# Kernel tuning notes

Hardware: AMD Instinct MI355X
Metric: run time of the kernel (lower is better)

## Reference

```python
import jax, jax.numpy as jnp
import numpy as np

HIDDEN = 2048
NUM_HEADS = 16
HEAD_DIM = HIDDEN // NUM_HEADS
ROPE_THETA = 10000.0


def _rope_cos_sin(n, dtype):
    # Llama-style: inv_freq over even indices, emb = concat([freqs, freqs])
    inv_freq = 1.0 / (ROPE_THETA ** (jnp.arange(0, HEAD_DIM, 2, dtype=jnp.float32) / HEAD_DIM))
    pos = jnp.arange(n, dtype=jnp.float32)
    freqs = pos[:, None] * inv_freq[None, :]          # [N, HEAD_DIM/2]
    emb = jnp.concatenate([freqs, freqs], axis=-1)    # [N, HEAD_DIM]
    return jnp.cos(emb).astype(dtype), jnp.sin(emb).astype(dtype)


def _rotate_half(x):
    x1, x2 = jnp.split(x, 2, axis=-1)
    return jnp.concatenate([-x2, x1], axis=-1)


def setup_inputs() -> dict:
    key = jax.random.key(0)
    ks = jax.random.split(key, 5)
    B, N, D = 2, 2048, HIDDEN
    s = 1.0 / np.sqrt(D)
    return {
        "x": jax.random.normal(ks[0], (B, N, D), jnp.float32),
        "Wq": jax.random.normal(ks[1], (D, D), jnp.float32) * s,
        "Wk": jax.random.normal(ks[2], (D, D), jnp.float32) * s,
        "Wv": jax.random.normal(ks[3], (D, D), jnp.float32) * s,
        "Wo": jax.random.normal(ks[4], (D, D), jnp.float32) * s,
    }


def reference(x, Wq, Wk, Wv, Wo):
    B, N, D = x.shape
    scale = HEAD_DIM ** -0.5

    def proj(W):  # nn.Linear(bias=False): x @ W.T, then split heads -> [B,H,N,hd]
        return (x @ W.T).reshape(B, N, NUM_HEADS, HEAD_DIM).transpose(0, 2, 1, 3)

    q, k, v = proj(Wq), proj(Wk), proj(Wv)

    cos, sin = _rope_cos_sin(N, x.dtype)  # [N, HEAD_DIM]
    cos = cos[None, None]                 # broadcast over B, H
    sin = sin[None, None]
    q = q * cos + _rotate_half(q) * sin
    k = k * cos + _rotate_half(k) * sin

    attn = jnp.einsum("bhqd,bhkd->bhqk", q, k) * scale  # full N x N scores
    attn = jax.nn.softmax(attn, axis=-1)                 # dropout p=0 -> identity
    out = jnp.einsum("bhqk,bhkd->bhqd", attn, v)
    out = out.transpose(0, 2, 1, 3).reshape(B, N, D)
    return out @ Wo.T
```

## Files before the change

### kernel.cpp

```cpp
#include <hip/hip_runtime.h>
#include <hip/hip_bf16.h>
#include <math.h>

typedef short bf16x8 __attribute__((ext_vector_type(8)));
typedef short bf16x4 __attribute__((ext_vector_type(4)));
typedef float f32x4 __attribute__((ext_vector_type(4)));

#define NSEQ 2048
#define DMODEL 2048
#define NH 16
#define HD 128
#define BATCH 2
#define MROWS 4096

__device__ __forceinline__ unsigned short f2b(float f) {
    __hip_bfloat16 h = __float2bfloat16(f);
    return *reinterpret_cast<unsigned short*>(&h);
}
__device__ __forceinline__ float b2f(unsigned short u) {
    __hip_bfloat16 h;
    *reinterpret_cast<unsigned short*>(&h) = u;
    return __bfloat162float(h);
}

__device__ __forceinline__ void gld_lds16(const unsigned short* g, unsigned short* l) {
    __builtin_amdgcn_global_load_lds(
        (const __attribute__((address_space(1))) unsigned int*)(const void*)g,
        (__attribute__((address_space(3))) unsigned int*)(void*)l,
        16, 0, 0);
}

__global__ __launch_bounds__(256) void cast_all_kernel(const float* __restrict__ x,
                                                       const float* __restrict__ wq,
                                                       const float* __restrict__ wk,
                                                       const float* __restrict__ wv,
                                                       const float* __restrict__ wo,
                                                       unsigned short* __restrict__ xb,
                                                       unsigned short* __restrict__ wqb) {
    int bid = blockIdx.x;
    const float* src;
    unsigned short* dst;
    int off;
    if (bid < 4096) {
        src = x; dst = xb; off = bid;
    } else {
        int w = (bid - 4096) >> 11;
        src = (w == 0) ? wq : (w == 1) ? wk : (w == 2) ? wv : wo;
        dst = wqb + (size_t)w * 4194304;
        off = (bid - 4096) & 2047;
    }
    int i = (off * 256 + threadIdx.x) * 8;
    float4 a = *(const float4*)(src + i);
    float4 b = *(const float4*)(src + i + 4);
    union { unsigned short u[8]; uint4 v; } tmp;
    tmp.u[0] = f2b(a.x); tmp.u[1] = f2b(a.y); tmp.u[2] = f2b(a.z); tmp.u[3] = f2b(a.w);
    tmp.u[4] = f2b(b.x); tmp.u[5] = f2b(b.y); tmp.u[6] = f2b(b.z); tmp.u[7] = f2b(b.w);
    *(uint4*)(dst + i) = tmp.v;
}

__global__ __launch_bounds__(256) void gemm_qkv(const unsigned short* __restrict__ A,
                                                const unsigned short* __restrict__ Bw,
                                                unsigned short* __restrict__ qk,
                                                unsigned short* __restrict__ vt) {
    __shared__ unsigned short sA[128 * 32];
    __shared__ unsigned short sB[128 * 32];
    const int K = DMODEL;
    const int tid = threadIdx.x;
    const int wave = tid >> 6, lane = tid & 63;
    const int m0 = blockIdx.y * 128, n0 = blockIdx.x * 128;
    const int wm = (wave >> 1) * 64, wn = (wave & 1) * 64;

    f32x4 acc[4][4] = {};

    const int srow = wave * 32 + (lane >> 2);
    const int scol = (lane & 3) * 8;
    const unsigned short* Ag = A + (size_t)(m0 + srow) * K + scol;
    const unsigned short* Bg = Bw + (size_t)(n0 + srow) * K + scol;
    unsigned short* sA0 = &sA[(wave * 32) * 32];
    unsigned short* sA1 = &sA[(wave * 32 + 16) * 32];
    unsigned short* sB0 = &sB[(wave * 32) * 32];
    unsigned short* sB1 = &sB[(wave * 32 + 16) * 32];
    const int fr = lane & 15, fo = (lane >> 4) * 8;

    for (int kb = 0; kb < K; kb += 32) {
        gld_lds16(Ag + kb, sA0);
        gld_lds16(Ag + (size_t)16 * K + kb, sA1);
        gld_lds16(Bg + kb, sB0);
        gld_lds16(Bg + (size_t)16 * K + kb, sB1);
        __syncthreads();
        bf16x8 af[4], bfr[4];
        #pragma unroll
        for (int mt = 0; mt < 4; mt++)
            af[mt] = *(const bf16x8*)&sA[(wm + mt * 16 + fr) * 32 + fo];
        #pragma unroll
        for (int nt = 0; nt < 4; nt++)
            bfr[nt] = *(const bf16x8*)&sB[(wn + nt * 16 + fr) * 32 + fo];
        #pragma unroll
        for (int mt = 0; mt < 4; mt++)
            #pragma unroll
            for (int nt = 0; nt < 4; nt++)
                acc[mt][nt] = __builtin_amdgcn_mfma_f32_16x16x32_bf16(af[mt], bfr[nt], acc[mt][nt], 0, 0, 0);
        __syncthreads();
    }

    const int g4 = (lane >> 4) * 4, c0 = lane & 15;
    if (n0 < 4096) {
        #pragma unroll
        for (int mt = 0; mt < 4; mt++)
            #pragma unroll
            for (int nt = 0; nt < 4; nt++) {
                int col = n0 + wn + nt * 16 + c0;
                size_t base = (size_t)(col >> 11) * 8388608 + (size_t)(col & 2047);
                #pragma unroll
                for (int r = 0; r < 4; r++) {
                    int row = m0 + wm + mt * 16 + g4 + r;
                    qk[base + (size_t)row * 2048] = f2b(acc[mt][nt][r]);
                }
            }
    } else {
        #pragma unroll
        for (int mt = 0; mt < 4; mt++) {
            int mbase = m0 + wm + mt * 16 + g4;
            int bb = mbase >> 11;
            int nn = mbase & 2047;
            #pragma unroll
            for (int nt = 0; nt < 4; nt++) {
                int d = n0 - 4096 + wn + nt * 16 + c0;
                union { unsigned short u[4]; uint2 v; } o;
                #pragma unroll
                for (int r = 0; r < 4; r++) o.u[r] = f2b(acc[mt][nt][r]);
                *(uint2*)(vt + ((size_t)(bb * 2048 + d)) * 2048 + nn) = o.v;
            }
        }
    }
}

__global__ __launch_bounds__(256) void gemm_out(const unsigned short* __restrict__ A,
                                                const unsigned short* __restrict__ Bw,
                                                float* __restrict__ Cf) {
    __shared__ unsigned short sA[128 * 32];
    __shared__ unsigned short sB[128 * 32];
    const int K = DMODEL, Nn = DMODEL;
    const int tid = threadIdx.x;
    const int wave = tid >> 6, lane = tid & 63;
    const int m0 = blockIdx.y * 128, n0 = blockIdx.x * 128;
    const int wm = (wave >> 1) * 64, wn = (wave & 1) * 64;

    f32x4 acc[4][4] = {};

    const int srow = wave * 32 + (lane >> 2);
    const int scol = (lane & 3) * 8;
    const unsigned short* Ag = A + (size_t)(m0 + srow) * K + scol;
    const unsigned short* Bg = Bw + (size_t)(n0 + srow) * K + scol;
    unsigned short* sA0 = &sA[(wave * 32) * 32];
    unsigned short* sA1 = &sA[(wave * 32 + 16) * 32];
    unsigned short* sB0 = &sB[(wave * 32) * 32];
    unsigned short* sB1 = &sB[(wave * 32 + 16) * 32];
    const int fr = lane & 15, fo = (lane >> 4) * 8;

    for (int kb = 0; kb < K; kb += 32) {
        gld_lds16(Ag + kb, sA0);
        gld_lds16(Ag + (size_t)16 * K + kb, sA1);
        gld_lds16(Bg + kb, sB0);
        gld_lds16(Bg + (size_t)16 * K + kb, sB1);
        __syncthreads();
        bf16x8 af[4], bfr[4];
        #pragma unroll
        for (int mt = 0; mt < 4; mt++)
            af[mt] = *(const bf16x8*)&sA[(wm + mt * 16 + fr) * 32 + fo];
        #pragma unroll
        for (int nt = 0; nt < 4; nt++)
            bfr[nt] = *(const bf16x8*)&sB[(wn + nt * 16 + fr) * 32 + fo];
        #pragma unroll
        for (int mt = 0; mt < 4; mt++)
            #pragma unroll
            for (int nt = 0; nt < 4; nt++)
                acc[mt][nt] = __builtin_amdgcn_mfma_f32_16x16x32_bf16(af[mt], bfr[nt], acc[mt][nt], 0, 0, 0);
        __syncthreads();
    }

    const int g4 = (lane >> 4) * 4, c0 = lane & 15;
    #pragma unroll
    for (int mt = 0; mt < 4; mt++)
        #pragma unroll
        for (int nt = 0; nt < 4; nt++) {
            int col = n0 + wn + nt * 16 + c0;
            #pragma unroll
            for (int r = 0; r < 4; r++) {
                int row = m0 + wm + mt * 16 + g4 + r;
                Cf[(size_t)row * Nn + col] = acc[mt][nt][r];
            }
        }
}

__global__ __launch_bounds__(256) void rope_kernel(unsigned short* __restrict__ Q,
                                                   unsigned short* __restrict__ Kb) {
    int t = blockIdx.x * 256 + threadIdx.x;
    int dq = t & 15, h = (t >> 4) & 15, m = t >> 8;
    int n = m & (NSEQ - 1);
    size_t base = (size_t)m * DMODEL + h * HD + dq * 4;

    union U4 { unsigned short u[4]; uint2 v; };
    U4 qlo, qhi, klo, khi, oql, oqh, okl, okh;
    qlo.v = *(const uint2*)(Q + base);
    qhi.v = *(const uint2*)(Q + base + 64);
    klo.v = *(const uint2*)(Kb + base);
    khi.v = *(const uint2*)(Kb + base + 64);

    const float scq = 0.08838834764831845f;
    #pragma unroll
    for (int j = 0; j < 4; j++) {
        int d = dq * 4 + j;
        float invf = exp2f((float)d * -0.2076205059304545f);
        float fr = (float)n * invf;
        float sv, cv;
        __sincosf(fr, &sv, &cv);
        float q1 = b2f(qlo.u[j]), q2 = b2f(qhi.u[j]);
        float k1 = b2f(klo.u[j]), k2 = b2f(khi.u[j]);
        oql.u[j] = f2b((q1 * cv - q2 * sv) * scq);
        oqh.u[j] = f2b((q2 * cv + q1 * sv) * scq);
        okl.u[j] = f2b(k1 * cv - k2 * sv);
        okh.u[j] = f2b(k2 * cv + k1 * sv);
    }
    *(uint2*)(Q + base)       = oql.v;
    *(uint2*)(Q + base + 64)  = oqh.v;
    *(uint2*)(Kb + base)      = okl.v;
    *(uint2*)(Kb + base + 64) = okh.v;
}

__global__ __launch_bounds__(256) void attn_kernel(const unsigned short* __restrict__ Q,
                                                   const unsigned short* __restrict__ Kg,
                                                   const unsigned short* __restrict__ Vt,
                                                   unsigned short* __restrict__ O) {
    __shared__ unsigned short sK[64 * 136];
    __shared__ unsigned short sV[128 * 88];

    const int bh = blockIdx.x;
    const int b = bh >> 4, h = bh & 15;
    const int qt = blockIdx.y;
    const int tid = threadIdx.x, wave = tid >> 6, lane = tid & 63;
    const int c0 = lane & 15, grp = lane >> 4;

    bf16x8 qf[2][4];
    {
        const unsigned short* Qbase = Q + (size_t)(b * NSEQ + qt * 128 + wave * 32 + c0) * DMODEL + h * HD + grp * 8;
        #pragma unroll
        for (int nt = 0; nt < 2; nt++)
            #pragma unroll
            for (int ks = 0; ks < 4; ks++)
                qf[nt][ks] = *(const bf16x8*)(Qbase + (size_t)nt * 16 * DMODEL + ks * 32);
    }

    f32x4 oacc[8][2] = {};
    float lsum[2] = {0.f, 0.f};

    const unsigned short* Kbase = Kg + (size_t)(b * NSEQ) * DMODEL + h * HD;
    const unsigned short* Vbase = Vt + (size_t)(bh * HD) * NSEQ;

    for (int kv0 = 0; kv0 < NSEQ; kv0 += 64) {
        __syncthreads();
        #pragma unroll
        for (int i = 0; i < 4; i++) {
            int fl = i * 256 + tid;
            int rr = fl >> 4, cc = fl & 15;
            *(uint4*)&sK[rr * 136 + cc * 8] = *(const uint4*)(Kbase + (size_t)(kv0 + rr) * DMODEL + cc * 8);
        }
        #pragma unroll
        for (int i = 0; i < 4; i++) {
            int fl = i * 256 + tid;
            int rr = fl >> 3, cc = fl & 7;
            *(uint4*)&sV[rr * 88 + cc * 8] = *(const uint4*)(Vbase + (size_t)rr * NSEQ + kv0 + cc * 8);
        }
        __syncthreads();

        f32x4 s[4][2] = {};
        #pragma unroll
        for (int ks = 0; ks < 4; ks++) {
            bf16x8 kf[4];
            #pragma unroll
            for (int mt = 0; mt < 4; mt++)
                kf[mt] = *(const bf16x8*)&sK[(mt * 16 + c0) * 136 + ks * 32 + grp * 8];
            #pragma unroll
            for (int mt = 0; mt < 4; mt++)
                #pragma unroll
                for (int nt = 0; nt < 2; nt++)
                    s[mt][nt] = __builtin_amdgcn_mfma_f32_16x16x32_bf16(kf[mt], qf[nt][ks], s[mt][nt], 0, 0, 0);
        }

        bf16x4 pk[4][2];
        #pragma unroll
        for (int mt = 0; mt < 4; mt++)
            #pragma unroll
            for (int nt = 0; nt < 2; nt++) {
                float p0 = __expf(s[mt][nt][0]);
                float p1 = __expf(s[mt][nt][1]);
                float p2 = __expf(s[mt][nt][2]);
                float p3 = __expf(s[mt][nt][3]);
                lsum[nt] += (p0 + p1) + (p2 + p3);
                bf16x4 t;
                t[0] = (short)f2b(p0); t[1] = (short)f2b(p1);
                t[2] = (short)f2b(p2); t[3] = (short)f2b(p3);
                pk[mt][nt] = t;
            }

        #pragma unroll
        for (int mtK = 0; mtK < 4; mtK++) {
            bf16x4 va[8];
            #pragma unroll
            for (int mo = 0; mo < 8; mo++)
                va[mo] = *(const bf16x4*)&sV[(mo * 16 + c0) * 88 + mtK * 16 + grp * 4];
            #pragma unroll
            for (int mo = 0; mo < 8; mo++)
                #pragma unroll
                for (int nt = 0; nt < 2; nt++)
                    oacc[mo][nt] = __builtin_amdgcn_mfma_f32_16x16x16bf16_1k(va[mo], pk[mtK][nt], oacc[mo][nt], 0, 0, 0);
        }
    }

    float invl[2];
    #pragma unroll
    for (int nt = 0; nt < 2; nt++) {
        float li = lsum[nt];
        li += __shfl_xor(li, 16);
        li += __shfl_xor(li, 32);
        invl[nt] = 1.0f / li;
    }
    #pragma unroll
    for (int mo = 0; mo < 8; mo++)
        #pragma unroll
        for (int nt = 0; nt < 2; nt++) {
            union { unsigned short u[4]; uint2 v; } o;
            #pragma unroll
            for (int r = 0; r < 4; r++)
                o.u[r] = f2b(oacc[mo][nt][r] * invl[nt]);
            int row = b * NSEQ + qt * 128 + wave * 32 + nt * 16 + c0;
            int col = h * HD + mo * 16 + grp * 4;
            *(uint2*)(O + (size_t)row * DMODEL + col) = o.v;
        }
}

extern "C" void kernel_launch(void* const* d_in, const int* in_sizes, int n_in,
                              void* d_out, int out_size, void* d_ws, size_t ws_size,
                              hipStream_t stream) {
    const float* x  = (const float*)d_in[0];
    const float* Wq = (const float*)d_in[1];
    const float* Wk = (const float*)d_in[2];
    const float* Wv = (const float*)d_in[3];
    const float* Wo = (const float*)d_in[4];

    char* ws = (char*)d_ws;
    unsigned short* xb  = (unsigned short*)(ws);
    unsigned short* wqb = (unsigned short*)(ws + 16777216);
    unsigned short* wob = (unsigned short*)(ws + 16777216 + 3 * 8388608);
    unsigned short* qb  = (unsigned short*)(ws + 50331648);
    unsigned short* kb  = (unsigned short*)(ws + 67108864);
    unsigned short* vt  = (unsigned short*)(ws + 83886080);

    cast_all_kernel<<<12288, 256, 0, stream>>>(x, Wq, Wk, Wv, Wo, xb, wqb);

    gemm_qkv<<<dim3(48, 32), 256, 0, stream>>>(xb, wqb, qb, vt);

    rope_kernel<<<4096, 256, 0, stream>>>(qb, kb);

    attn_kernel<<<dim3(32, 16), 256, 0, stream>>>(qb, kb, vt, xb);

    gemm_out<<<dim3(16, 32), 256, 0, stream>>>(xb, wob, (float*)d_out);
}
```

Before: 423.1 us.

## Fuse RoPE into QKV GEMM epilogue and shrink output GEMM M-tile

The QKV GEMM now gives each wave a full 128-column head slice (2x8 MFMA tiles), so the lo/hi halves needed by rotate_half sit in the same thread. RoPE and the Q scale are applied in the epilogue, which removes the separate rope kernel and its read-modify-write pass over Q and K. The output GEMM moves to 64-row tiles, doubling the grid to 1024 blocks to improve CU occupancy. The costs are more sincos work in the epilogue and less operand reuse per block in gemm_out.

```diff
diff --git a/kernel.cpp b/kernel.cpp
--- a/kernel.cpp
+++ b/kernel.cpp
@@ -68,9 +68,9 @@
     const int tid = threadIdx.x;
     const int wave = tid >> 6, lane = tid & 63;
     const int m0 = blockIdx.y * 128, n0 = blockIdx.x * 128;
-    const int wm = (wave >> 1) * 64, wn = (wave & 1) * 64;
-
-    f32x4 acc[4][4] = {};
+    const int wm = wave * 32;
+
+    f32x4 acc[2][8] = {};
 
     const int srow = wave * 32 + (lane >> 2);
     const int scol = (lane & 3) * 8;
@@ -88,44 +88,56 @@
         gld_lds16(Bg + kb, sB0);
         gld_lds16(Bg + (size_t)16 * K + kb, sB1);
         __syncthreads();
-        bf16x8 af[4], bfr[4];
-        #pragma unroll
-        for (int mt = 0; mt < 4; mt++)
+        bf16x8 af[2], bfr[8];
+        #pragma unroll
+        for (int mt = 0; mt < 2; mt++)
             af[mt] = *(const bf16x8*)&sA[(wm + mt * 16 + fr) * 32 + fo];
         #pragma unroll
-        for (int nt = 0; nt < 4; nt++)
-            bfr[nt] = *(const bf16x8*)&sB[(wn + nt * 16 + fr) * 32 + fo];
-        #pragma unroll
-        for (int mt = 0; mt < 4; mt++)
-            #pragma unroll
-            for (int nt = 0; nt < 4; nt++)
+        for (int nt = 0; nt < 8; nt++)
+            bfr[nt] = *(const bf16x8*)&sB[(nt * 16 + fr) * 32 + fo];
+        #pragma unroll
+        for (int mt = 0; mt < 2; mt++)
+            #pragma unroll
+            for (int nt = 0; nt < 8; nt++)
                 acc[mt][nt] = __builtin_amdgcn_mfma_f32_16x16x32_bf16(af[mt], bfr[nt], acc[mt][nt], 0, 0, 0);
         __syncthreads();
     }
 
     const int g4 = (lane >> 4) * 4, c0 = lane & 15;
     if (n0 < 4096) {
-        #pragma unroll
-        for (int mt = 0; mt < 4; mt++)
-            #pragma unroll
-            for (int nt = 0; nt < 4; nt++) {
-                int col = n0 + wn + nt * 16 + c0;
-                size_t base = (size_t)(col >> 11) * 8388608 + (size_t)(col & 2047);
+        const float scale = (n0 < 2048) ? 0.08838834764831845f : 1.0f;
+        unsigned short* dst = qk + (size_t)(n0 >> 11) * 8388608;
+        const int colbase = n0 & 2047;
+        float invf[4];
+        #pragma unroll
+        for (int nt = 0; nt < 4; nt++)
+            invf[nt] = exp2f((float)(nt * 16 + c0) * -0.2076205059304545f);
+        #pragma unroll
+        for (int mt = 0; mt < 2; mt++) {
+            #pragma unroll
+            for (int r = 0; r < 4; r++) {
+                int row = m0 + wm + mt * 16 + g4 + r;
+                float nf = (float)(row & (NSEQ - 1));
+                size_t rbase = (size_t)row * 2048 + colbase + c0;
                 #pragma unroll
-                for (int r = 0; r < 4; r++) {
-                    int row = m0 + wm + mt * 16 + g4 + r;
-                    qk[base + (size_t)row * 2048] = f2b(acc[mt][nt][r]);
+                for (int nt = 0; nt < 4; nt++) {
+                    float sv, cv;
+                    __sincosf(nf * invf[nt], &sv, &cv);
+                    float lo = acc[mt][nt][r], hi = acc[mt][nt + 4][r];
+                    dst[rbase + nt * 16]      = f2b((lo * cv - hi * sv) * scale);
+                    dst[rbase + nt * 16 + 64] = f2b((hi * cv + lo * sv) * scale);
                 }
             }
+        }
     } else {
         #pragma unroll
-        for (int mt = 0; mt < 4; mt++) {
+        for (int mt = 0; mt < 2; mt++) {
             int mbase = m0 + wm + mt * 16 + g4;
             int bb = mbase >> 11;
             int nn = mbase & 2047;
             #pragma unroll
-            for (int nt = 0; nt < 4; nt++) {
-                int d = n0 - 4096 + wn + nt * 16 + c0;
+            for (int nt = 0; nt < 8; nt++) {
+                int d = n0 - 4096 + nt * 16 + c0;
                 union { unsigned short u[4]; uint2 v; } o;
                 #pragma unroll
                 for (int r = 0; r < 4; r++) o.u[r] = f2b(acc[mt][nt][r]);
@@ -138,41 +150,40 @@
 __global__ __launch_bounds__(256) void gemm_out(const unsigned short* __restrict__ A,
                                                 const unsigned short* __restrict__ Bw,
                                                 float* __restrict__ Cf) {
-    __shared__ unsigned short sA[128 * 32];
+    __shared__ unsigned short sA[64 * 32];
     __shared__ unsigned short sB[128 * 32];
     const int K = DMODEL, Nn = DMODEL;
     const int tid = threadIdx.x;
     const int wave = tid >> 6, lane = tid & 63;
-    const int m0 = blockIdx.y * 128, n0 = blockIdx.x * 128;
-    const int wm = (wave >> 1) * 64, wn = (wave & 1) * 64;
-
-    f32x4 acc[4][4] = {};
-
-    const int srow = wave * 32 + (lane >> 2);
+    const int m0 = blockIdx.y * 64, n0 = blockIdx.x * 128;
+    const int wm = (wave >> 1) * 32, wn = (wave & 1) * 64;
+
+    f32x4 acc[2][4] = {};
+
+    const int srowA = wave * 16 + (lane >> 2);
+    const int srowB = wave * 32 + (lane >> 2);
     const int scol = (lane & 3) * 8;
-    const unsigned short* Ag = A + (size_t)(m0 + srow) * K + scol;
-    const unsigned short* Bg = Bw + (size_t)(n0 + srow) * K + scol;
-    unsigned short* sA0 = &sA[(wave * 32) * 32];
-    unsigned short* sA1 = &sA[(wave * 32 + 16) * 32];
+    const unsigned short* Ag = A + (size_t)(m0 + srowA) * K + scol;
+    const unsigned short* Bg = Bw + (size_t)(n0 + srowB) * K + scol;
+    unsigned short* sA0 = &sA[(wave * 16) * 32];
     unsigned short* sB0 = &sB[(wave * 32) * 32];
     unsigned short* sB1 = &sB[(wave * 32 + 16) * 32];
     const int fr = lane & 15, fo = (lane >> 4) * 8;
 
     for (int kb = 0; kb < K; kb += 32) {
         gld_lds16(Ag + kb, sA0);
-        gld_lds16(Ag + (size_t)16 * K + kb, sA1);
         gld_lds16(Bg + kb, sB0);
         gld_lds16(Bg + (size_t)16 * K + kb, sB1);
         __syncthreads();
-        bf16x8 af[4], bfr[4];
-        #pragma unroll
-        for (int mt = 0; mt < 4; mt++)
+        bf16x8 af[2], bfr[4];
+        #pragma unroll
+        for (int mt = 0; mt < 2; mt++)
             af[mt] = *(const bf16x8*)&sA[(wm + mt * 16 + fr) * 32 + fo];
         #pragma unroll
         for (int nt = 0; nt < 4; nt++)
             bfr[nt] = *(const bf16x8*)&sB[(wn + nt * 16 + fr) * 32 + fo];
         #pragma unroll
-        for (int mt = 0; mt < 4; mt++)
+        for (int mt = 0; mt < 2; mt++)
             #pragma unroll
             for (int nt = 0; nt < 4; nt++)
                 acc[mt][nt] = __builtin_amdgcn_mfma_f32_16x16x32_bf16(af[mt], bfr[nt], acc[mt][nt], 0, 0, 0);
@@ -181,7 +192,7 @@
 
     const int g4 = (lane >> 4) * 4, c0 = lane & 15;
     #pragma unroll
-    for (int mt = 0; mt < 4; mt++)
+    for (int mt = 0; mt < 2; mt++)
         #pragma unroll
         for (int nt = 0; nt < 4; nt++) {
             int col = n0 + wn + nt * 16 + c0;
@@ -191,41 +202,6 @@
                 Cf[(size_t)row * Nn + col] = acc[mt][nt][r];
             }
         }
-}
-
-__global__ __launch_bounds__(256) void rope_kernel(unsigned short* __restrict__ Q,
-                                                   unsigned short* __restrict__ Kb) {
-    int t = blockIdx.x * 256 + threadIdx.x;
-    int dq = t & 15, h = (t >> 4) & 15, m = t >> 8;
-    int n = m & (NSEQ - 1);
-    size_t base = (size_t)m * DMODEL + h * HD + dq * 4;
-
-    union U4 { unsigned short u[4]; uint2 v; };
-    U4 qlo, qhi, klo, khi, oql, oqh, okl, okh;
-    qlo.v = *(const uint2*)(Q + base);
-    qhi.v = *(const uint2*)(Q + base + 64);
-    klo.v = *(const uint2*)(Kb + base);
-    khi.v = *(const uint2*)(Kb + base + 64);
-
-    const float scq = 0.08838834764831845f;
-    #pragma unroll
-    for (int j = 0; j < 4; j++) {
-        int d = dq * 4 + j;
-        float invf = exp2f((float)d * -0.2076205059304545f);
-        float fr = (float)n * invf;
-        float sv, cv;
-        __sincosf(fr, &sv, &cv);
-        float q1 = b2f(qlo.u[j]), q2 = b2f(qhi.u[j]);
-        float k1 = b2f(klo.u[j]), k2 = b2f(khi.u[j]);
-        oql.u[j] = f2b((q1 * cv - q2 * sv) * scq);
-        oqh.u[j] = f2b((q2 * cv + q1 * sv) * scq);
-        okl.u[j] = f2b(k1 * cv - k2 * sv);
-        okh.u[j] = f2b(k2 * cv + k1 * sv);
-    }
-    *(uint2*)(Q + base)       = oql.v;
-    *(uint2*)(Q + base + 64)  = oqh.v;
-    *(uint2*)(Kb + base)      = okl.v;
-    *(uint2*)(Kb + base + 64) = okh.v;
 }
 
 __global__ __launch_bounds__(256) void attn_kernel(const unsigned short* __restrict__ Q,
@@ -360,9 +336,7 @@
 
     gemm_qkv<<<dim3(48, 32), 256, 0, stream>>>(xb, wqb, qb, vt);
 
-    rope_kernel<<<4096, 256, 0, stream>>>(qb, kb);
-
     attn_kernel<<<dim3(32, 16), 256, 0, stream>>>(qb, kb, vt, xb);
 
-    gemm_out<<<dim3(16, 32), 256, 0, stream>>>(xb, wob, (float*)d_out);
-}
+    gemm_out<<<dim3(16, 64), 256, 0, stream>>>(xb, wob, (float*)d_out);
+}
```

Result: no change. 414.8 us (-2.0%).
